# Kernel tuning notes

Hardware: AMD Instinct MI355X
Metric: run time of the kernel (lower is better)

Reference implementation:

```python
import jax, jax.numpy as jnp
import numpy as np

B, C, N = 4, 128, 8192
CQK = C // 4  # query/key projection dim = out_channels // 4


def setup_inputs() -> dict:
    key = jax.random.key(0)
    ks = jax.random.split(key, 9)
    s_in = 1.0 / np.sqrt(C)
    return {
        "x": jax.random.normal(ks[0], (B, C, N), dtype=jnp.float32),
        "xyz": jax.random.normal(ks[1], (B, N, 3), dtype=jnp.float32),
        "Wq": jax.random.normal(ks[2], (CQK, C), dtype=jnp.float32) * s_in,
        "bq": jax.random.normal(ks[3], (CQK,), dtype=jnp.float32) * 0.01,
        "Wk": jax.random.normal(ks[4], (CQK, C), dtype=jnp.float32) * s_in,
        "bk": jax.random.normal(ks[5], (CQK,), dtype=jnp.float32) * 0.01,
        "Wv": jax.random.normal(ks[6], (C, C), dtype=jnp.float32) * s_in,
        "bv": jax.random.normal(ks[7], (C,), dtype=jnp.float32) * 0.01,
        "gamma": jax.random.normal(ks[8], (1,), dtype=jnp.float32) * 0.1,
    }


def reference(x, xyz, Wq, bq, Wk, bk, Wv, bv, gamma):
    # 1x1 Conv1d == per-point linear projection over channels
    q = jnp.einsum('oc,bcn->bon', Wq, x) + bq[None, :, None]   # (B, CQK, N)
    k = jnp.einsum('oc,bcn->bon', Wk, x) + bk[None, :, None]   # (B, CQK, N)
    v = jnp.einsum('oc,bcn->bon', Wv, x) + bv[None, :, None]   # (B, C, N)

    # energy[b, n, m] = <q[:, n], k[:, m]>
    energy = jnp.einsum('bcn,bcm->bnm', q, k)                  # (B, N, N)

    # positional correlation bias: normalize coords per point, cosine-sim matrix
    xyz_bcn = jnp.swapaxes(xyz, 1, 2)                          # (B, 3, N)
    xyz_norm = xyz_bcn / (jnp.linalg.norm(xyz_bcn, axis=1, keepdims=True) + 1e-8)
    pos_corr = jnp.einsum('bcn,bcm->bnm', xyz_norm, xyz_norm)  # (B, N, N)
    energy = energy + 0.1 * pos_corr

    attention = jax.nn.softmax(energy, axis=-1)                # rowwise over m

    # out[b, c, n] = sum_m v[b, c, m] * attention[b, n, m]
    out = jnp.einsum('bcm,bnm->bcn', v, attention)             # (B, C, N)
    return gamma * out + x
```

## Files before the change

### kernel.cpp

```cpp
#include <hip/hip_runtime.h>

#define NPTS 8192
#define NB 4
#define NCH 128
#define DQK 48
#define TK 64
#define SPLIT 4
#define KEYS_PER (NPTS / SPLIT)
#define ROUNDS (KEYS_PER / TK)
#define SH2 28.853901f
#define LOG2E 1.4426950408889634f

typedef unsigned short ushort_t;
typedef unsigned int uint_t;
typedef __attribute__((ext_vector_type(8))) short bf16x8;
typedef __attribute__((ext_vector_type(4))) float f32x4;
typedef __attribute__((ext_vector_type(16))) float f32x16;

static __device__ __forceinline__ ushort_t f2bf(float x) {
  union { float f; uint_t u; } v; v.f = x;
  uint_t r = v.u + 0x7fffu + ((v.u >> 16) & 1u);
  return (ushort_t)(r >> 16);
}
static __device__ __forceinline__ float bf2f(ushort_t u) {
  union { uint_t i; float f; } v; v.i = ((uint_t)u) << 16; return v.f;
}
static __device__ __forceinline__ int sig16(int n) {
  int g2 = (n >> 2) & 3;
  return (g2 == 1 || g2 == 2) ? (n ^ 0xC) : n;
}

typedef __attribute__((address_space(1))) void void_g;
typedef __attribute__((address_space(3))) void void_l;
static __device__ __forceinline__ void gload_lds16(const ushort_t* g, ushort_t* l) {
  __builtin_amdgcn_global_load_lds((void_g*)(ushort_t*)g, (void_l*)l, 16, 0, 0);
}

__global__ __launch_bounds__(512, 1)
void wprep_kernel(const float* __restrict__ Wq, const float* __restrict__ bq,
                  const float* __restrict__ Wk, const float* __restrict__ bk,
                  const float* __restrict__ Wv, const float* __restrict__ bv,
                  ushort_t* __restrict__ Wb, float* __restrict__ bias_pre) {
  const int z = blockIdx.x;
  const int ks = threadIdx.x >> 6;
  const int lane = threadIdx.x & 63;
  const int l31 = lane & 31, h = lane >> 5;
  const float* W = (z == 0) ? Wq : (z == 1) ? Wk : (Wv + (size_t)(z - 2) * 32 * 128);
  const float sc = (z == 0) ? LOG2E : 1.0f;
  const float* wr = W + l31 * 128 + ks * 16 + h * 8;
  union { ushort_t u[8]; bf16x8 v; } p;
#pragma unroll
  for (int j = 0; j < 8; ++j) p.u[j] = f2bf(wr[j] * sc);
  *(bf16x8*)(Wb + ((size_t)(z * 8 + ks) * 64 + lane) * 8) = p.v;
  if (z == 0 && threadIdx.x < 192) {
    int i = threadIdx.x;
    bias_pre[i] = (i < 32) ? bq[i] * LOG2E : (i < 64) ? bk[i - 32] : bv[i - 64];
  }
}

__global__ __launch_bounds__(256, 4)
void projm2_kernel(const float* __restrict__ x, const float* __restrict__ xyz,
                   const ushort_t* __restrict__ Wb,
                   const float* __restrict__ bias_pre,
                   ushort_t* __restrict__ Qb, ushort_t* __restrict__ Kb,
                   ushort_t* __restrict__ Vt) {
  const int tid = threadIdx.x;
  const int lane = tid & 63, wv = tid >> 6;
  const int l31 = lane & 31, h = lane >> 5;
  const int b = blockIdx.y;
  const int n = blockIdx.x * 128 + wv * 32 + l31;

  bf16x8 bfr[8];
  const float* xb = x + (size_t)b * NCH * NPTS + n;
#pragma unroll
  for (int ks = 0; ks < 8; ++ks) {
    const float* xc = xb + (size_t)(ks * 16 + h * 8) * NPTS;
    union { ushort_t u[8]; bf16x8 v; } p;
#pragma unroll
    for (int j = 0; j < 8; ++j) p.u[j] = f2bf(xc[(size_t)j * NPTS]);
    bfr[ks] = p.v;
  }

  float xa = xyz[((size_t)b * NPTS + n) * 3 + 0];
  float xc2 = xyz[((size_t)b * NPTS + n) * 3 + 1];
  float xd = xyz[((size_t)b * NPTS + n) * 3 + 2];
  float rinv = 1.0f / (sqrtf(xa * xa + xc2 * xc2 + xd * xd) + 1e-8f);

#pragma unroll 1
  for (int z = 0; z < 6; ++z) {
    f32x16 S;
#pragma unroll
    for (int r = 0; r < 16; ++r)
      S[r] = bias_pre[z * 32 + (r & 3) + 8 * (r >> 2) + 4 * h];
#pragma unroll
    for (int ks = 0; ks < 8; ++ks) {
      bf16x8 af = *(const bf16x8*)(Wb + ((size_t)(z * 8 + ks) * 64 + lane) * 8);
      S = __builtin_amdgcn_mfma_f32_32x32x16_bf16(af, bfr[ks], S, 0, 0, 0);
    }
    if (z <= 1) {
      float sc = (z == 0) ? LOG2E : 1.0f;
      ushort_t* dst = (z == 0 ? Qb : Kb) + ((size_t)b * NPTS + n) * DQK;
#pragma unroll
      for (int r = 0; r < 16; ++r)
        dst[(r & 3) + 8 * (r >> 2) + 4 * h] = f2bf(S[r]);
      float rn = 0.31622776601683794f * sc * rinv;
      union { ushort_t u[16]; bf16x8 v[2]; } t;
#pragma unroll
      for (int j = 0; j < 16; ++j) t.u[j] = 0;
      t.u[0] = f2bf(xa * rn); t.u[1] = f2bf(xc2 * rn); t.u[2] = f2bf(xd * rn);
      t.u[3] = (z == 0) ? f2bf(-SH2) : f2bf(1.0f);
      *(bf16x8*)(dst + 32) = t.v[0];
      *(bf16x8*)(dst + 40) = t.v[1];
    } else {
      const int np = (n & ~15) | sig16(n & 15);
      const int c0 = (z - 2) * 32;
#pragma unroll
      for (int r = 0; r < 16; ++r)
        Vt[((size_t)b * NCH + c0 + (r & 3) + 8 * (r >> 2) + 4 * h) * NPTS + np] =
            f2bf(S[r]);
    }
  }
}

__global__ __launch_bounds__(512, 4)
void attn32_kernel(const ushort_t* __restrict__ Qb, const ushort_t* __restrict__ Kb,
                   const ushort_t* __restrict__ Vt,
                   ushort_t* __restrict__ PACC, float* __restrict__ PL) {
  __shared__ __align__(16) ushort_t L[2][22][512];
  const int tid = threadIdx.x;
  const int lane = tid & 63, w = tid >> 6;
  const int l31 = lane & 31, h = lane >> 5;

  const int lin = blockIdx.x;
  const int bs = lin & 15;
  const int b = bs & 3, sseg = bs >> 2;
  const int qblk = lin >> 4;
  const int q0w = qblk * 256 + w * 32;
  const int m00 = sseg * KEYS_PER;

  bf16x8 qf[3];
#pragma unroll
  for (int c = 0; c < 3; ++c)
    qf[c] = *(const bf16x8*)(Qb + ((size_t)b * NPTS + q0w + l31) * DQK +
                             c * 16 + h * 8);

  const ushort_t* gp[3];
  int fid[3], adv[3];
  const int nf = (w < 6) ? 3 : 2;
#pragma unroll
  for (int i = 0; i < 3; ++i) {
    int fi = w + 8 * i;
    fid[i] = fi;
    if (fi < 6) {
      int kb = fi / 3, c = fi - kb * 3;
      gp[i] = Kb + ((size_t)b * NPTS + m00 + kb * 32 + l31) * DQK + c * 16 + h * 8;
      adv[i] = TK * DQK;
    } else if (fi < 22) {
      int vi = fi - 6, fch = vi >> 2, kk = vi & 3;
      gp[i] = Vt + ((size_t)b * NCH + fch * 32 + l31) * NPTS + m00 + kk * 16 + h * 8;
      adv[i] = TK;
    }
  }

  f32x16 O[4];
#pragma unroll
  for (int f = 0; f < 4; ++f) O[f] = (f32x16)(0.f);
  float ls0 = 0.f, ls1 = 0.f;

#pragma unroll
  for (int i = 0; i < 3; ++i)
    if (i < nf) gload_lds16(gp[i], &L[0][fid[i]][0]);

#pragma unroll 1
  for (int t = 0; t < ROUNDS; ++t) {
    __syncthreads();
    const int cur = t & 1;
    if (t + 1 < ROUNDS) {
#pragma unroll
      for (int i = 0; i < 3; ++i)
        if (i < nf) {
          gp[i] += adv[i];
          gload_lds16(gp[i], &L[cur ^ 1][fid[i]][0]);
        }
    }

#pragma unroll
    for (int kb = 0; kb < 2; ++kb) {
      bf16x8 kf0 = *(const bf16x8*)(&L[cur][kb * 3 + 0][0] + lane * 8);
      bf16x8 kf1 = *(const bf16x8*)(&L[cur][kb * 3 + 1][0] + lane * 8);
      bf16x8 kf2 = *(const bf16x8*)(&L[cur][kb * 3 + 2][0] + lane * 8);

      __builtin_amdgcn_s_setprio(1);
      f32x16 S = __builtin_amdgcn_mfma_f32_32x32x16_bf16(kf0, qf[0],
                                                         (f32x16)(0.f), 0, 0, 0);
      S = __builtin_amdgcn_mfma_f32_32x32x16_bf16(kf1, qf[1], S, 0, 0, 0);
      S = __builtin_amdgcn_mfma_f32_32x32x16_bf16(kf2, qf[2], S, 0, 0, 0);
      __builtin_amdgcn_s_setprio(0);

      uint_t pk[8];
#pragma unroll
      for (int i = 0; i < 8; ++i) {
        float p0 = __builtin_amdgcn_exp2f(S[2 * i]);
        float p1 = __builtin_amdgcn_exp2f(S[2 * i + 1]);
        ls0 += p0;
        ls1 += p1;
        pk[i] = __builtin_amdgcn_perm(__float_as_uint(p1), __float_as_uint(p0),
                                      0x07060302u);
      }

#pragma unroll
      for (int kkl = 0; kkl < 2; ++kkl) {
        union { uint_t u[4]; bf16x8 v; } au;
        au.u[0] = pk[4 * kkl + 0];
        au.u[1] = pk[4 * kkl + 1];
        au.u[2] = pk[4 * kkl + 2];
        au.u[3] = pk[4 * kkl + 3];
        bf16x8 A = au.v;
        __builtin_amdgcn_s_setprio(1);
#pragma unroll
        for (int f = 0; f < 4; ++f) {
          bf16x8 vf = *(const bf16x8*)(&L[cur][6 + f * 4 + kb * 2 + kkl][0] + lane * 8);
          O[f] = __builtin_amdgcn_mfma_f32_32x32x16_bf16(A, vf, O[f], 0, 0, 0);
        }
        __builtin_amdgcn_s_setprio(0);
      }
    }
  }

  float lsum = ls0 + ls1;
  lsum += __shfl_xor(lsum, 32);
  const size_t pbase = (size_t)(bs * 16 + (qblk >> 1)) * 16 + (qblk & 1) * 8 + w;
#pragma unroll
  for (int f = 0; f < 4; ++f) {
    union { ushort_t u[16]; bf16x8 v[2]; } pu;
#pragma unroll
    for (int r = 0; r < 16; ++r) pu.u[r] = f2bf(O[f][r]);
    size_t idx = (pbase * 4 + f) * 1024 + (size_t)lane * 16;
    *(bf16x8*)(PACC + idx) = pu.v[0];
    *(bf16x8*)(PACC + idx + 8) = pu.v[1];
  }
  if (lane < 32) PL[(size_t)bs * NPTS + q0w + lane] = lsum;
}

#define MPITCH 268
__global__ __launch_bounds__(256, 4)
void merge4c_kernel(const ushort_t* __restrict__ PACC, const float* __restrict__ PL,
                    const float* __restrict__ x, const float* __restrict__ gamma,
                    float* __restrict__ out) {
  __shared__ float Linv[256];
  __shared__ float ldso[32 * MPITCH];
  const int tid = threadIdx.x;
  const int qblk2 = blockIdx.x, b = blockIdx.y, f = blockIdx.z;
  const int q0 = qblk2 * 256;

  float Ls = 0.f;
#pragma unroll
  for (int s = 0; s < 4; ++s)
    Ls += PL[(size_t)(s * 4 + b) * NPTS + q0 + tid];
  Linv[tid] = gamma[0] / Ls;
  __syncthreads();

  const int ww = tid >> 6, lane = tid & 63, l31 = lane & 31, h = lane >> 5;

#pragma unroll
  for (int g = 0; g < 2; ++g) {
    float acc[16];
#pragma unroll
    for (int r = 0; r < 16; ++r) acc[r] = 0.f;
#pragma unroll
    for (int s = 0; s < 4; ++s) {
      size_t idx = (((((size_t)(s * 4 + b) * 16 + (qblk2 >> 1)) * 8 +
                      (qblk2 & 1) * 4 + ww) * 2 + g) * 4 + f) * 1024 +
                   (size_t)lane * 16;
      bf16x8 a0 = *(const bf16x8*)(PACC + idx);
      bf16x8 a1 = *(const bf16x8*)(PACC + idx + 8);
#pragma unroll
      for (int r = 0; r < 8; ++r) {
        acc[r] += bf2f((ushort_t)a0[r]);
        acc[8 + r] += bf2f((ushort_t)a1[r]);
      }
    }
    const int qb = ww * 64 + g * 32 + 4 * h;
#pragma unroll
    for (int rr = 0; rr < 4; ++rr) {
      int q = qb + 8 * rr;
      f32x4 v;
#pragma unroll
      for (int i = 0; i < 4; ++i) v[i] = acc[rr * 4 + i] * Linv[q + i];
      *(f32x4*)&ldso[l31 * MPITCH + q] = v;
    }
  }
  __syncthreads();

  const float* xb = x + ((size_t)b * NCH + f * 32) * NPTS + q0;
  float* ob = out + ((size_t)b * NCH + f * 32) * NPTS + q0;
#pragma unroll
  for (int rr = 0; rr < 8; ++rr) {
    int ch = ww * 8 + rr;
    f32x4 v = *(const f32x4*)&ldso[ch * MPITCH + lane * 4];
    f32x4 xv = *(const f32x4*)(xb + (size_t)ch * NPTS + lane * 4);
    v += xv;
    *(f32x4*)(ob + (size_t)ch * NPTS + lane * 4) = v;
  }
}

extern "C" void kernel_launch(void* const* d_in, const int* in_sizes, int n_in,
                              void* d_out, int out_size, void* d_ws,
                              size_t ws_size, hipStream_t stream) {
  const float* x     = (const float*)d_in[0];
  const float* xyz   = (const float*)d_in[1];
  const float* Wq    = (const float*)d_in[2];
  const float* bq    = (const float*)d_in[3];
  const float* Wk    = (const float*)d_in[4];
  const float* bk    = (const float*)d_in[5];
  const float* Wv    = (const float*)d_in[6];
  const float* bv    = (const float*)d_in[7];
  const float* gamma = (const float*)d_in[8];
  float* out = (float*)d_out;

  const size_t BN = (size_t)NB * NPTS;
  ushort_t* Qb = (ushort_t*)d_ws;
  ushort_t* Kb = Qb + BN * DQK;
  ushort_t* Vt = Kb + BN * DQK;
  ushort_t* PACC = Vt + BN * NCH;
  float* PL = (float*)(PACC + (size_t)16 * 16 * 8 * 2 * 4 * 1024);
  ushort_t* Wb = (ushort_t*)(PL + 16 * BN / 2);
  float* bias_pre = (float*)(Wb + 6 * 8 * 64 * 8);

  wprep_kernel<<<6, 512, 0, stream>>>(Wq, bq, Wk, bk, Wv, bv, Wb, bias_pre);
  projm2_kernel<<<dim3(NPTS / 128, NB), 256, 0, stream>>>(
      x, xyz, Wb, bias_pre, Qb, Kb, Vt);
  attn32_kernel<<<512, 512, 0, stream>>>(Qb, Kb, Vt, PACC, PL);
  merge4c_kernel<<<dim3(32, NB, 4), 256, 0, stream>>>(PACC, PL, x, gamma, out);
  (void)in_sizes; (void)n_in; (void)out_size; (void)ws_size;
}
```

Baseline: 190.6 us.

## Store Q/K/V in MFMA-fragment-tiled layout via LDS transpose in projection

The projection kernel now stages its outputs through a per-wave LDS tile and writes Q, K and V in a pre-tiled layout of 512-element fragment blocks. Each load the attention kernel issues is then one contiguous 1KB chunk instead of strided rows. This is meant to coalesce the scattered 2-byte stores in projection and the strided global-to-LDS loads in attention. The cost is extra LDS traffic in projection, and the producer and consumer index mappings must stay exactly consistent.

```diff
diff --git a/kernel.cpp b/kernel.cpp
--- a/kernel.cpp
+++ b/kernel.cpp
@@ -35,6 +35,7 @@
 static __device__ __forceinline__ void gload_lds16(const ushort_t* g, ushort_t* l) {
   __builtin_amdgcn_global_load_lds((void_g*)(ushort_t*)g, (void_l*)l, 16, 0, 0);
 }
+
 
 __global__ __launch_bounds__(512, 1)
 void wprep_kernel(const float* __restrict__ Wq, const float* __restrict__ bq,
@@ -58,17 +59,20 @@
   }
 }
 
+#define TPITCH 40
 __global__ __launch_bounds__(256, 4)
 void projm2_kernel(const float* __restrict__ x, const float* __restrict__ xyz,
                    const ushort_t* __restrict__ Wb,
                    const float* __restrict__ bias_pre,
                    ushort_t* __restrict__ Qb, ushort_t* __restrict__ Kb,
                    ushort_t* __restrict__ Vt) {
+  __shared__ __align__(16) ushort_t T[4][32 * TPITCH];
   const int tid = threadIdx.x;
   const int lane = tid & 63, wv = tid >> 6;
   const int l31 = lane & 31, h = lane >> 5;
   const int b = blockIdx.y;
-  const int n = blockIdx.x * 128 + wv * 32 + l31;
+  const int n0 = blockIdx.x * 128 + wv * 32;
+  const int n = n0 + l31;
 
   bf16x8 bfr[8];
   const float* xb = x + (size_t)b * NCH * NPTS + n;
@@ -86,6 +90,9 @@
   float xd = xyz[((size_t)b * NPTS + n) * 3 + 2];
   float rinv = 1.0f / (sqrtf(xa * xa + xc2 * xc2 + xd * xd) + 1e-8f);
 
+  const int nploc = (l31 & 16) | sig16(l31 & 15);
+  ushort_t* tw = &T[wv][0];
+
 #pragma unroll 1
   for (int z = 0; z < 6; ++z) {
     f32x16 S;
@@ -98,26 +105,37 @@
       S = __builtin_amdgcn_mfma_f32_32x32x16_bf16(af, bfr[ks], S, 0, 0, 0);
     }
     if (z <= 1) {
+#pragma unroll
+      for (int r = 0; r < 16; ++r)
+        tw[l31 * TPITCH + (r & 3) + 8 * (r >> 2) + 4 * h] = f2bf(S[r]);
+      ushort_t* dstf = (z == 0 ? Qb : Kb) +
+                       (((size_t)b * 256 + (n0 >> 5)) * 3) * 512;
+#pragma unroll
+      for (int c = 0; c < 2; ++c) {
+        bf16x8 fr = *(const bf16x8*)&tw[(lane & 31) * TPITCH + c * 16 + (lane >> 5) * 8];
+        *(bf16x8*)(dstf + c * 512 + lane * 8) = fr;
+      }
       float sc = (z == 0) ? LOG2E : 1.0f;
-      ushort_t* dst = (z == 0 ? Qb : Kb) + ((size_t)b * NPTS + n) * DQK;
-#pragma unroll
-      for (int r = 0; r < 16; ++r)
-        dst[(r & 3) + 8 * (r >> 2) + 4 * h] = f2bf(S[r]);
       float rn = 0.31622776601683794f * sc * rinv;
       union { ushort_t u[16]; bf16x8 v[2]; } t;
 #pragma unroll
       for (int j = 0; j < 16; ++j) t.u[j] = 0;
       t.u[0] = f2bf(xa * rn); t.u[1] = f2bf(xc2 * rn); t.u[2] = f2bf(xd * rn);
       t.u[3] = (z == 0) ? f2bf(-SH2) : f2bf(1.0f);
-      *(bf16x8*)(dst + 32) = t.v[0];
-      *(bf16x8*)(dst + 40) = t.v[1];
+      *(bf16x8*)(dstf + 1024 + l31 * 8) = t.v[0];
+      *(bf16x8*)(dstf + 1024 + 256 + l31 * 8) = t.v[1];
     } else {
-      const int np = (n & ~15) | sig16(n & 15);
-      const int c0 = (z - 2) * 32;
 #pragma unroll
       for (int r = 0; r < 16; ++r)
-        Vt[((size_t)b * NCH + c0 + (r & 3) + 8 * (r >> 2) + 4 * h) * NPTS + np] =
-            f2bf(S[r]);
+        tw[((r & 3) + 8 * (r >> 2) + 4 * h) * TPITCH + nploc] = f2bf(S[r]);
+#pragma unroll
+      for (int g = 0; g < 2; ++g) {
+        bf16x8 fr = *(const bf16x8*)&tw[(lane & 31) * TPITCH + g * 16 + (lane >> 5) * 8];
+        int kk = ((n0 >> 4) + g) & 3;
+        ushort_t* dst = Vt + ((((size_t)b * 128 + (n0 >> 6)) * 16 +
+                               (z - 2) * 4 + kk) * 512);
+        *(bf16x8*)(dst + lane * 8) = fr;
+      }
     }
   }
 }
@@ -129,7 +147,6 @@
   __shared__ __align__(16) ushort_t L[2][22][512];
   const int tid = threadIdx.x;
   const int lane = tid & 63, w = tid >> 6;
-  const int l31 = lane & 31, h = lane >> 5;
 
   const int lin = blockIdx.x;
   const int bs = lin & 15;
@@ -139,11 +156,14 @@
   const int m00 = sseg * KEYS_PER;
 
   bf16x8 qf[3];
-#pragma unroll
-  for (int c = 0; c < 3; ++c)
-    qf[c] = *(const bf16x8*)(Qb + ((size_t)b * NPTS + q0w + l31) * DQK +
-                             c * 16 + h * 8);
-
+  {
+    const ushort_t* qbase = Qb + (((size_t)b * 256 + (q0w >> 5)) * 3) * 512 + lane * 8;
+#pragma unroll
+    for (int c = 0; c < 3; ++c) qf[c] = *(const bf16x8*)(qbase + c * 512);
+  }
+
+  const ushort_t* vbase = Vt + (((size_t)b * 128 + (m00 >> 6)) * 16) * 512 + lane * 8;
+  const ushort_t* kbase = Kb + (((size_t)b * 256 + (m00 >> 5)) * 3) * 512 + lane * 8;
   const ushort_t* gp[3];
   int fid[3], adv[3];
   const int nf = (w < 6) ? 3 : 2;
@@ -151,15 +171,8 @@
   for (int i = 0; i < 3; ++i) {
     int fi = w + 8 * i;
     fid[i] = fi;
-    if (fi < 6) {
-      int kb = fi / 3, c = fi - kb * 3;
-      gp[i] = Kb + ((size_t)b * NPTS + m00 + kb * 32 + l31) * DQK + c * 16 + h * 8;
-      adv[i] = TK * DQK;
-    } else if (fi < 22) {
-      int vi = fi - 6, fch = vi >> 2, kk = vi & 3;
-      gp[i] = Vt + ((size_t)b * NCH + fch * 32 + l31) * NPTS + m00 + kk * 16 + h * 8;
-      adv[i] = TK;
-    }
+    if (fi < 16) { gp[i] = vbase + fi * 512; adv[i] = 16 * 512; }
+    else if (fi < 22) { gp[i] = kbase + (fi - 16) * 512; adv[i] = 6 * 512; }
   }
 
   f32x16 O[4];
@@ -186,9 +199,9 @@
 
 #pragma unroll
     for (int kb = 0; kb < 2; ++kb) {
-      bf16x8 kf0 = *(const bf16x8*)(&L[cur][kb * 3 + 0][0] + lane * 8);
-      bf16x8 kf1 = *(const bf16x8*)(&L[cur][kb * 3 + 1][0] + lane * 8);
-      bf16x8 kf2 = *(const bf16x8*)(&L[cur][kb * 3 + 2][0] + lane * 8);
+      bf16x8 kf0 = *(const bf16x8*)(&L[cur][16 + kb * 3 + 0][0] + lane * 8);
+      bf16x8 kf1 = *(const bf16x8*)(&L[cur][16 + kb * 3 + 1][0] + lane * 8);
+      bf16x8 kf2 = *(const bf16x8*)(&L[cur][16 + kb * 3 + 2][0] + lane * 8);
 
       __builtin_amdgcn_s_setprio(1);
       f32x16 S = __builtin_amdgcn_mfma_f32_32x32x16_bf16(kf0, qf[0],
@@ -219,7 +232,7 @@
         __builtin_amdgcn_s_setprio(1);
 #pragma unroll
         for (int f = 0; f < 4; ++f) {
-          bf16x8 vf = *(const bf16x8*)(&L[cur][6 + f * 4 + kb * 2 + kkl][0] + lane * 8);
+          bf16x8 vf = *(const bf16x8*)(&L[cur][f * 4 + kb * 2 + kkl][0] + lane * 8);
           O[f] = __builtin_amdgcn_mfma_f32_32x32x16_bf16(A, vf, O[f], 0, 0, 0);
         }
         __builtin_amdgcn_s_setprio(0);
```

After: 189.2 us. Within noise of the previous version (-0.7%).
